# Optimization experiments

Hardware: AMD Instinct MI355X
Metric: run time of the kernel (lower is better)

## Reference

```python
import jax, jax.numpy as jnp
import numpy as np

D_MODEL = 512
N_HEADS = 8
POI_N, POI_F = 1683, 24


def _linear_params(k, fan_in, fan_out):
    kw, kb = jax.random.split(k)
    bound = 1.0 / np.sqrt(fan_in)
    w = jax.random.uniform(kw, (fan_in, fan_out), jnp.float32, -bound, bound)
    b = jax.random.uniform(kb, (fan_out,), jnp.float32, -bound, bound)
    return w, b


def setup_inputs() -> dict:
    key = jax.random.key(0)
    ks = jax.random.split(key, 7)
    B, L, D = 8, 8192, D_MODEL
    x = jax.random.normal(ks[0], (B, L, D), jnp.float32)
    poi_data = jax.random.normal(ks[1], (POI_N, POI_F), jnp.float32)
    wq1, bq1 = _linear_params(ks[2], POI_F, 1)
    wq2, bq2 = _linear_params(ks[3], POI_N, D)
    wk, bk = _linear_params(ks[4], D, D)
    wv, bv = _linear_params(ks[5], D, D)
    wo, bo = _linear_params(ks[6], D, D)
    return dict(x=x, poi_data=poi_data, wq1=wq1, bq1=bq1, wq2=wq2, bq2=bq2,
                wk=wk, bk=bk, wv=wv, bv=bv, wo=wo, bo=bo)


def reference(x, poi_data, wq1, bq1, wq2, bq2, wk, bk, wv, bv, wo, bo):
    B, L, D = x.shape
    H = N_HEADS
    d = D // H
    # key / value projections: [B, L, H, d]
    k = (x @ wk + bk).reshape(B, L, H, d)
    v = (x @ wv + bv).reshape(B, L, H, d)
    # query: Linear(24,1) over poi features, squeeze, Linear(1683, d_model)
    q = (poi_data @ wq1 + bq1)[:, 0]          # [1683]
    q = (q @ wq2 + bq2).reshape(H, d)         # [H, d] -- shared across B and L
    scale = 1.0 / jnp.sqrt(jnp.asarray(d, x.dtype))
    # Original computes scores [B,H,L,L] where every row l is identical
    # (query is broadcast over L). Mathematically equivalent collapsed form:
    scores = jnp.einsum('he,bshe->bhs', q, k)  # [B, H, L]
    A = jax.nn.softmax(scale * scores, axis=-1)
    V = jnp.einsum('bhs,bshd->bhd', A, v).reshape(B, H * d)  # [B, D]
    out = jnp.broadcast_to(V[:, None, :], (B, L, H * d))      # same row for all L
    return out @ wo + bo
```

## Files before the change

### kernel.cpp

```cpp
#include <hip/hip_runtime.h>
#include <math.h>

#define L_SEQ 8192
#define B_N   8

typedef float f4v __attribute__((ext_vector_type(4)));

#define QKV_OFF    0
#define V_OFF      4096
#define ROW_OFF    8192
#define QFP_OFF    12288
#define DPART_OFF  40960
#define YPART_OFF  65536

__global__ __launch_bounds__(512) void k2_qf(const float* __restrict__ poi,
                                             const float* __restrict__ wq1,
                                             const float* __restrict__ bq1,
                                             const float* __restrict__ wq2, float* ws) {
    __shared__ float qr[32];
    int k = blockIdx.x, t = threadIdx.x;
    int i0 = k * 32;
    int cnt = 1683 - i0; if (cnt > 32) cnt = 32;
    if (t < cnt) {
        float a = bq1[0];
#pragma unroll
        for (int j = 0; j < 24; ++j) a += poi[(i0 + t) * 24 + j] * wq1[j];
        qr[t] = a;
    }
    __syncthreads();
    float a = 0.f;
    for (int ii = 0; ii < cnt; ++ii) a += qr[ii] * wq2[(size_t)(i0 + ii) * 512 + t];
    ws[QFP_OFF + k * 512 + t] = a;
}

__global__ void k3_qkvec(const float* __restrict__ wk, const float* __restrict__ bq2,
                         const float* __restrict__ bv, const float* __restrict__ bo, float* ws) {
    __shared__ float qf[512];
    int t = threadIdx.x, bid = blockIdx.x;
    for (int o = t; o < 512; o += 256) {
        float s = bq2[o];
        for (int k = 0; k < 53; ++k) s += ws[QFP_OFF + k * 512 + o];
        qf[o] = s;
    }
    __syncthreads();
    int idx = bid * 256 + t;
    int h = idx >> 9, c = idx & 511;
    float a = 0.f;
#pragma unroll 8
    for (int e = 0; e < 64; ++e) a += qf[h * 64 + e] * wk[(size_t)c * 512 + h * 64 + e];
    ws[QKV_OFF + idx] = 0.125f * a;
    if (bid < 8) {
        ws[V_OFF + bid * 512 + t]       = bv[t];
        ws[V_OFF + bid * 512 + 256 + t] = bv[256 + t];
    } else {
        int b = bid - 8;
        ws[ROW_OFF + b * 512 + t]       = bo[t];
        ws[ROW_OFF + b * 512 + 256 + t] = bo[256 + t];
    }
}

__global__ __launch_bounds__(512) void kF(const float* __restrict__ x, float* __restrict__ ws) {
    __shared__ float qk_s[4096];
    __shared__ float num_s[4096];
    __shared__ float den_s[8];
    int t = threadIdx.x;
    int lane = t & 63, w = t >> 6;
    int b = blockIdx.x >> 6, slot = blockIdx.x & 63;
    int wslot = slot * 8 + w;

    {
        float4* qs4 = (float4*)qk_s;
        const float4* qg4 = (const float4*)(ws + QKV_OFF);
        qs4[t]       = qg4[t];
        qs4[t + 512] = qg4[t + 512];
    }
    __syncthreads();

    const int b0 = lane & 1, b1 = (lane >> 1) & 1, b2 = (lane >> 2) & 1;
    float num[8][8] = {{0.f}};
    float den_own = 0.f;

    const float4* xp = (const float4*)(x + (size_t)b * L_SEQ * 512);
    const float4* qk4 = (const float4*)qk_s;
    float4 cxa = xp[(size_t)wslot * 128 + lane * 2];
    float4 cxb = xp[(size_t)wslot * 128 + lane * 2 + 1];

    for (int r = wslot; r < L_SEQ; r += 512) {
        int rn = r + 512;
        float4 nxa = cxa, nxb = cxb;
        if (rn < L_SEQ) {
            nxa = xp[(size_t)rn * 128 + lane * 2];
            nxb = xp[(size_t)rn * 128 + lane * 2 + 1];
        }
        float p[8];
#pragma unroll
        for (int h = 0; h < 8; ++h) {
            float4 qa = qk4[h * 128 + lane * 2];
            float4 qb = qk4[h * 128 + lane * 2 + 1];
            p[h] = cxa.x * qa.x + cxa.y * qa.y + cxa.z * qa.z + cxa.w * qa.w
                 + cxb.x * qb.x + cxb.y * qb.y + cxb.z * qb.z + cxb.w * qb.w;
        }
        float v0, v1, v2, v3, u0, u1, s;
        {
            float k0 = b0 ? p[1] : p[0], s0 = b0 ? p[0] : p[1];
            float k1 = b0 ? p[3] : p[2], s1 = b0 ? p[2] : p[3];
            float k2 = b0 ? p[5] : p[4], s2 = b0 ? p[4] : p[5];
            float k3 = b0 ? p[7] : p[6], s3 = b0 ? p[6] : p[7];
            v0 = k0 + __shfl_xor(s0, 1, 64);
            v1 = k1 + __shfl_xor(s1, 1, 64);
            v2 = k2 + __shfl_xor(s2, 1, 64);
            v3 = k3 + __shfl_xor(s3, 1, 64);
        }
        {
            float k0 = b1 ? v1 : v0, s0 = b1 ? v0 : v1;
            float k1 = b1 ? v3 : v2, s1 = b1 ? v2 : v3;
            u0 = k0 + __shfl_xor(s0, 2, 64);
            u1 = k1 + __shfl_xor(s1, 2, 64);
        }
        {
            float k0 = b2 ? u1 : u0, s0 = b2 ? u0 : u1;
            s = k0 + __shfl_xor(s0, 4, 64);
        }
        s += __shfl_xor(s, 8, 64);
        s += __shfl_xor(s, 16, 64);
        s += __shfl_xor(s, 32, 64);
        float wg1 = __expf(s);
        den_own += wg1;
        float wg[8];
#pragma unroll
        for (int h = 0; h < 8; ++h) wg[h] = __shfl(wg1, h, 64);
#pragma unroll
        for (int h = 0; h < 8; ++h) {
            num[h][0] += wg[h] * cxa.x; num[h][1] += wg[h] * cxa.y;
            num[h][2] += wg[h] * cxa.z; num[h][3] += wg[h] * cxa.w;
            num[h][4] += wg[h] * cxb.x; num[h][5] += wg[h] * cxb.y;
            num[h][6] += wg[h] * cxb.z; num[h][7] += wg[h] * cxb.w;
        }
        cxa = nxa; cxb = nxb;
    }

    for (int wi = 0; wi < 8; ++wi) {
        if (w == wi) {
#pragma unroll
            for (int h = 0; h < 8; ++h) {
                int base = h * 512 + lane * 8;
                if (wi == 0) {
#pragma unroll
                    for (int j = 0; j < 8; ++j) num_s[base + j] = num[h][j];
                } else {
#pragma unroll
                    for (int j = 0; j < 8; ++j) num_s[base + j] += num[h][j];
                }
            }
            if (lane < 8) { if (wi == 0) den_s[lane] = den_own; else den_s[lane] += den_own; }
        }
        __syncthreads();
    }
    float4* yp4 = (float4*)(ws + YPART_OFF + (size_t)blockIdx.x * 4096);
    const float4* ns4 = (const float4*)num_s;
    yp4[t]       = ns4[t];
    yp4[512 + t] = ns4[512 + t];
    if (t < 8) ws[DPART_OFF + blockIdx.x * 8 + t] = den_s[t];
}

__global__ __launch_bounds__(512) void kV(const float* __restrict__ wv, float* ws) {
    __shared__ float red[512];
    __shared__ float yn_s[512];
    __shared__ float dinv[8];
    int b = blockIdx.x >> 3, cc = blockIdx.x & 7;
    int c0 = cc * 64;
    int t = threadIdx.x;
    red[t] = ws[DPART_OFF + (size_t)(b * 64 + (t >> 3)) * 8 + (t & 7)];
    __syncthreads();
#pragma unroll
    for (int off = 256; off >= 8; off >>= 1) {
        if (t < off) red[t] += red[t + off];
        __syncthreads();
    }
    if (t < 8) dinv[t] = 1.f / red[t];
    int h = t >> 6, cl = t & 63;
    float s = 0.f;
    const float* yp = ws + YPART_OFF + (size_t)(b * 64) * 4096 + h * 512 + c0 + cl;
#pragma unroll 8
    for (int sl = 0; sl < 64; ++sl) s += yp[(size_t)sl * 4096];
    __syncthreads();
    yn_s[t] = s * dinv[h];
    __syncthreads();
    int o = t, ho = o >> 6;
    const float* yh = yn_s + ho * 64;
    float acc = 0.f;
#pragma unroll 8
    for (int ci = 0; ci < 64; ++ci) acc += yh[ci] * wv[(size_t)(c0 + ci) * 512 + o];
    atomicAdd(ws + V_OFF + b * 512 + o, acc);
}

__global__ __launch_bounds__(512) void kRow(const float* __restrict__ wo, float* ws) {
    __shared__ float V_s[64];
    int b = blockIdx.x >> 3, oc = blockIdx.x & 7;
    int o0 = oc * 64;
    int t = threadIdx.x;
    if (t < 64) V_s[t] = ws[V_OFF + b * 512 + o0 + t];
    __syncthreads();
    float acc = 0.f;
#pragma unroll 8
    for (int oi = 0; oi < 64; ++oi) acc += V_s[oi] * wo[(size_t)(o0 + oi) * 512 + t];
    atomicAdd(ws + ROW_OFF + b * 512 + t, acc);
}

__global__ __launch_bounds__(256) void k9_out(const float* __restrict__ ws, float* __restrict__ out) {
    const f4v* row4 = (const f4v*)(ws + ROW_OFF);
    f4v* out4 = (f4v*)out;
    size_t stride = (size_t)gridDim.x * blockDim.x;
    for (size_t g = (size_t)blockIdx.x * blockDim.x + threadIdx.x; g < 8388608ull; g += stride) {
        int b = (int)(g >> 20);
        int q = (int)(g & 127);
        f4v v = row4[b * 128 + q];
        __builtin_nontemporal_store(v, &out4[g]);
    }
}

extern "C" void kernel_launch(void* const* d_in, const int* in_sizes, int n_in,
                              void* d_out, int out_size, void* d_ws, size_t ws_size,
                              hipStream_t stream) {
    const float* x   = (const float*)d_in[0];
    const float* poi = (const float*)d_in[1];
    const float* wq1 = (const float*)d_in[2];
    const float* bq1 = (const float*)d_in[3];
    const float* wq2 = (const float*)d_in[4];
    const float* bq2 = (const float*)d_in[5];
    const float* wk  = (const float*)d_in[6];
    const float* bk  = (const float*)d_in[7];
    const float* wv  = (const float*)d_in[8];
    const float* bv  = (const float*)d_in[9];
    const float* wo  = (const float*)d_in[10];
    const float* bo  = (const float*)d_in[11];
    float* ws  = (float*)d_ws;
    float* out = (float*)d_out;
    (void)bk;

    k2_qf<<<53, 512, 0, stream>>>(poi, wq1, bq1, wq2, ws);
    k3_qkvec<<<16, 256, 0, stream>>>(wk, bq2, bv, bo, ws);
    kF<<<512, 512, 0, stream>>>(x, ws);
    kV<<<64, 512, 0, stream>>>(wv, ws);
    kRow<<<64, 512, 0, stream>>>(wo, ws);
    k9_out<<<2048, 256, 0, stream>>>(ws, out);
}
```

Before: 93.05 us.

## Hold query vectors in registers, drop prefetch, shrink kF grid to 384 blocks

The fused score/accumulate kernel now loads each lane's slice of the per-head qk vectors into registers once, instead of staging them in shared memory and rereading them every row. The software prefetch of the next x row is removed. The grid drops from 512 to 384 blocks (48 per batch, 384-row stride), and the reduction kernel is adjusted to sum 48 partials. This removes LDS traffic and a barrier, and one-block-per-CU sizing is meant to avoid a tail wave. The costs are 64 extra VGPRs per thread, which may cut occupancy, and loss of the explicit load/compute overlap.

```diff
diff --git a/kernel.cpp b/kernel.cpp
--- a/kernel.cpp
+++ b/kernel.cpp
@@ -60,46 +60,37 @@
 }
 
 __global__ __launch_bounds__(512) void kF(const float* __restrict__ x, float* __restrict__ ws) {
-    __shared__ float qk_s[4096];
     __shared__ float num_s[4096];
     __shared__ float den_s[8];
     int t = threadIdx.x;
     int lane = t & 63, w = t >> 6;
-    int b = blockIdx.x >> 6, slot = blockIdx.x & 63;
+    int b = blockIdx.x / 48, slot = blockIdx.x % 48;
     int wslot = slot * 8 + w;
 
+    float4 qa[8], qb[8];
     {
-        float4* qs4 = (float4*)qk_s;
         const float4* qg4 = (const float4*)(ws + QKV_OFF);
-        qs4[t]       = qg4[t];
-        qs4[t + 512] = qg4[t + 512];
-    }
-    __syncthreads();
+#pragma unroll
+        for (int h = 0; h < 8; ++h) {
+            qa[h] = qg4[h * 128 + lane * 2];
+            qb[h] = qg4[h * 128 + lane * 2 + 1];
+        }
+    }
 
     const int b0 = lane & 1, b1 = (lane >> 1) & 1, b2 = (lane >> 2) & 1;
     float num[8][8] = {{0.f}};
     float den_own = 0.f;
 
     const float4* xp = (const float4*)(x + (size_t)b * L_SEQ * 512);
-    const float4* qk4 = (const float4*)qk_s;
-    float4 cxa = xp[(size_t)wslot * 128 + lane * 2];
-    float4 cxb = xp[(size_t)wslot * 128 + lane * 2 + 1];
-
-    for (int r = wslot; r < L_SEQ; r += 512) {
-        int rn = r + 512;
-        float4 nxa = cxa, nxb = cxb;
-        if (rn < L_SEQ) {
-            nxa = xp[(size_t)rn * 128 + lane * 2];
-            nxb = xp[(size_t)rn * 128 + lane * 2 + 1];
-        }
+
+    for (int r = wslot; r < L_SEQ; r += 384) {
+        float4 cxa = xp[(size_t)r * 128 + lane * 2];
+        float4 cxb = xp[(size_t)r * 128 + lane * 2 + 1];
         float p[8];
 #pragma unroll
-        for (int h = 0; h < 8; ++h) {
-            float4 qa = qk4[h * 128 + lane * 2];
-            float4 qb = qk4[h * 128 + lane * 2 + 1];
-            p[h] = cxa.x * qa.x + cxa.y * qa.y + cxa.z * qa.z + cxa.w * qa.w
-                 + cxb.x * qb.x + cxb.y * qb.y + cxb.z * qb.z + cxb.w * qb.w;
-        }
+        for (int h = 0; h < 8; ++h)
+            p[h] = cxa.x * qa[h].x + cxa.y * qa[h].y + cxa.z * qa[h].z + cxa.w * qa[h].w
+                 + cxb.x * qb[h].x + cxb.y * qb[h].y + cxb.z * qb[h].z + cxb.w * qb[h].w;
         float v0, v1, v2, v3, u0, u1, s;
         {
             float k0 = b0 ? p[1] : p[0], s0 = b0 ? p[0] : p[1];
@@ -136,7 +127,6 @@
             num[h][4] += wg[h] * cxb.x; num[h][5] += wg[h] * cxb.y;
             num[h][6] += wg[h] * cxb.z; num[h][7] += wg[h] * cxb.w;
         }
-        cxa = nxa; cxb = nxb;
     }
 
     for (int wi = 0; wi < 8; ++wi) {
@@ -170,7 +160,7 @@
     int b = blockIdx.x >> 3, cc = blockIdx.x & 7;
     int c0 = cc * 64;
     int t = threadIdx.x;
-    red[t] = ws[DPART_OFF + (size_t)(b * 64 + (t >> 3)) * 8 + (t & 7)];
+    red[t] = (t < 384) ? ws[DPART_OFF + (size_t)(b * 48 + (t >> 3)) * 8 + (t & 7)] : 0.f;
     __syncthreads();
 #pragma unroll
     for (int off = 256; off >= 8; off >>= 1) {
@@ -180,9 +170,9 @@
     if (t < 8) dinv[t] = 1.f / red[t];
     int h = t >> 6, cl = t & 63;
     float s = 0.f;
-    const float* yp = ws + YPART_OFF + (size_t)(b * 64) * 4096 + h * 512 + c0 + cl;
-#pragma unroll 8
-    for (int sl = 0; sl < 64; ++sl) s += yp[(size_t)sl * 4096];
+    const float* yp = ws + YPART_OFF + (size_t)(b * 48) * 4096 + h * 512 + c0 + cl;
+#pragma unroll 8
+    for (int sl = 0; sl < 48; ++sl) s += yp[(size_t)sl * 4096];
     __syncthreads();
     yn_s[t] = s * dinv[h];
     __syncthreads();
@@ -240,7 +230,7 @@
 
     k2_qf<<<53, 512, 0, stream>>>(poi, wq1, bq1, wq2, ws);
     k3_qkvec<<<16, 256, 0, stream>>>(wk, bq2, bv, bo, ws);
-    kF<<<512, 512, 0, stream>>>(x, ws);
+    kF<<<384, 512, 0, stream>>>(x, ws);
     kV<<<64, 512, 0, stream>>>(wv, ws);
     kRow<<<64, 512, 0, stream>>>(wo, ws);
     k9_out<<<2048, 256, 0, stream>>>(ws, out);
```

Result: slower. 107.2 us (+15.3%).
